# Performance work log

Hardware: AMD Instinct MI355X
Metric: run time of the kernel (lower is better)

The kernel has to match this reference:

```python
import jax, jax.numpy as jnp
import numpy as np

TOKEN_SELF_ATTN_VALUE = -5e4  # reformer_pytorch constant for masking self-attention
BUCKET_SIZE = 64
N_HASHES = 4
HEADS = 8


def look_one_back(x):
    # concat each chunk with the previous chunk along the within-chunk axis (axis=2)
    prev = jnp.concatenate([x[:, -1:], x[:, :-1]], axis=1)
    return jnp.concatenate([prev, x], axis=2)


def lsh_attention(qk, v, rotations):
    # qk, v: (b*h, t, dh); rotations: (dh, n_hashes, n_buckets//2)
    bh, seqlen, dim = qk.shape
    n_buckets = seqlen // BUCKET_SIZE
    # --- LSH bucket hashing via random rotations ---
    rotated = jnp.einsum('btf,fhi->bhti', qk, rotations)            # (bh, H, t, nb/2)
    rotated = jnp.concatenate([rotated, -rotated], axis=-1)          # (bh, H, t, nb)
    buckets = jnp.argmax(rotated, axis=-1)                           # (bh, H, t)
    offsets = (jnp.arange(N_HASHES) * n_buckets)[None, :, None]
    buckets = (buckets + offsets).reshape(bh, N_HASHES * seqlen)
    # --- stable sort tokens by (bucket, position) ---
    ticker = jnp.arange(N_HASHES * seqlen)
    buckets_and_t = seqlen * buckets + (ticker % seqlen)[None, :]
    sticker = jnp.argsort(buckets_and_t, axis=-1)                    # sorted ticker
    undo_sort = jnp.argsort(sticker, axis=-1)
    st = sticker % seqlen                                            # original positions
    sqk = jnp.take_along_axis(qk, st[..., None], axis=1)
    sv = jnp.take_along_axis(v, st[..., None], axis=1)
    # --- chunk into n_hashes*n_buckets chunks of bucket_size tokens ---
    n_chunks = N_HASHES * n_buckets
    bq_t = st.reshape(bh, n_chunks, -1)
    bqk = sqk.reshape(bh, n_chunks, -1, dim)
    bv = sv.reshape(bh, n_chunks, -1, dim)
    bq = bqk
    bk = bqk / jnp.maximum(jnp.linalg.norm(bqk, axis=-1, keepdims=True), 1e-12)
    bk = look_one_back(bk)
    bv = look_one_back(bv)
    bkv_t = look_one_back(bq_t)
    # --- chunked attention with one-chunk lookback ---
    dots = jnp.einsum('bcie,bcje->bcij', bq, bk) * (dim ** -0.5)     # (bh, nc, bs, 2*bs)
    dots = jnp.where(bq_t[:, :, :, None] == bkv_t[:, :, None, :], TOKEN_SELF_ATTN_VALUE, dots)
    dots_lse = jax.nn.logsumexp(dots, axis=-1, keepdims=True)
    probs = jnp.exp(dots - dots_lse)
    bo = jnp.einsum('bcij,bcje->bcie', probs, bv)
    so = bo.reshape(bh, N_HASHES * seqlen, dim)
    slogits = dots_lse.reshape(bh, N_HASHES * seqlen)
    # --- unsort and combine hash rounds weighted by logsumexp ---
    o = jnp.take_along_axis(so, undo_sort[..., None], axis=1)
    logits = jnp.take_along_axis(slogits, undo_sort, axis=1)
    o = o.reshape(bh, N_HASHES, seqlen, dim)
    logits = logits.reshape(bh, N_HASHES, seqlen, 1)
    w = jnp.exp(logits - jax.nn.logsumexp(logits, axis=1, keepdims=True))
    return jnp.sum(o * w, axis=1)


def _forward(queries, Wqk, Wv, Wo, bo, rotations):
    B, N, C = queries.shape
    m = BUCKET_SIZE * 2
    if N % m != 0:  # fit_length: zero-pad to multiple of bucket_size*2 (static)
        pad = m - N % m
        x = jnp.concatenate([queries, jnp.zeros((B, pad, C), queries.dtype)], axis=1)
    else:
        x = queries
    T = x.shape[1]
    dh = C // HEADS
    qk = jnp.einsum('btc,cf->btf', x, Wqk).reshape(B, T, HEADS, dh).transpose(0, 2, 1, 3).reshape(B * HEADS, T, dh)
    v = jnp.einsum('btc,cf->btf', x, Wv).reshape(B, T, HEADS, dh).transpose(0, 2, 1, 3).reshape(B * HEADS, T, dh)
    out = lsh_attention(qk, v, rotations)
    out = out.reshape(B, HEADS, T, dh).transpose(0, 2, 1, 3).reshape(B, T, C)
    out = jnp.einsum('btc,cf->btf', out, Wo) + bo
    return out[:, :N]


def setup_inputs() -> dict:
    key = jax.random.key(0)
    ks = jax.random.split(key, 7)
    B, N, C = 4, 4096, 512
    dh = C // HEADS
    n_buckets = N // BUCKET_SIZE  # 64
    return {
        'queries': jax.random.normal(ks[0], (B, N, C), jnp.float32),
        'keys': jax.random.normal(ks[1], (B, N, C), jnp.float32),
        'values': jax.random.normal(ks[2], (B, N, C), jnp.float32),
        'attn_mask': jnp.zeros((1,), jnp.bool_),
        'tau': 1,
        'delta': 1,
        'Wqk': jax.random.normal(ks[3], (C, C), jnp.float32) / np.float32(np.sqrt(C)),
        'Wv': jax.random.normal(ks[4], (C, C), jnp.float32) / np.float32(np.sqrt(C)),
        'Wo': jax.random.normal(ks[5], (C, C), jnp.float32) / np.float32(np.sqrt(C)),
        'bo': jnp.zeros((C,), jnp.float32),
        'rotations': jax.random.normal(ks[6], (dh, N_HASHES, n_buckets // 2), jnp.float32),
    }


def reference(queries, keys, values, attn_mask, tau, delta, Wqk, Wv, Wo, bo, rotations):
    # keys/values/attn_mask/tau/delta are accepted but unused, matching the torch module
    return _forward(queries, Wqk, Wv, Wo, bo, rotations)
```

## Files before the change

kernel.cpp:

```cpp
#include <hip/hip_runtime.h>
#include <hip/hip_bf16.h>
#include <cstdint>
#include <cstddef>

#define LSEQ   4096
#define DHD    64
#define NHASH  4
#define CDIM   512
#define NBH    32
#define MROWS  16384
#define NCHUNK 256

typedef __attribute__((ext_vector_type(8))) short short8;
typedef __attribute__((ext_vector_type(4))) float f32x4;
typedef __attribute__((ext_vector_type(2))) float f32x2;

__device__ inline uint32_t f2bf(float f) {
  uint32_t u = __float_as_uint(f);
  return (u + 0x7FFFu + ((u >> 16) & 1u)) >> 16;
}
__device__ inline float bf2f(uint32_t h) { return __uint_as_float(h << 16); }
__device__ inline void split2(float f, uint32_t& hi, uint32_t& lo) {
  hi = f2bf(f);
  lo = f2bf(f - bf2f(hi));
}
__device__ inline uint32_t cvtpk_bf16(float a, float b) {
  uint32_t r;
  asm("v_cvt_pk_bf16_f32 %0, %1, %2" : "=v"(r) : "v"(a), "v"(b));
  return r;
}
__device__ inline short8 ldsK(const uint16_t* p) {
  union { uint2 u[2]; short8 s; } t;
  t.u[0] = *reinterpret_cast<const uint2*>(p);
  t.u[1] = *reinterpret_cast<const uint2*>(p + 4);
  return t.s;
}

__global__ __launch_bounds__(256) void prep_kernel(
    const float* __restrict__ X, const float* __restrict__ Wv,
    const float* __restrict__ Wo,
    uint16_t* __restrict__ X0, uint16_t* __restrict__ X1,
    uint16_t* __restrict__ wvT0, uint16_t* __restrict__ wvT1,
    uint16_t* __restrict__ woT_hi, uint16_t* __restrict__ woT_lo)
{
  __shared__ float Ts[32][33];
  const int bid = blockIdx.x, tid = threadIdx.x;
  if (bid < 8192) {
    size_t i = ((size_t)bid * 256 + tid) * 4;
    float4 v = *reinterpret_cast<const float4*>(X + i);
    uint32_t h01 = cvtpk_bf16(v.x, v.y);
    uint32_t h23 = cvtpk_bf16(v.z, v.w);
    float r0 = v.x - __uint_as_float(h01 << 16);
    float r1 = v.y - __uint_as_float(h01 & 0xffff0000u);
    float r2 = v.z - __uint_as_float(h23 << 16);
    float r3 = v.w - __uint_as_float(h23 & 0xffff0000u);
    uint2 hw = {h01, h23};
    uint2 lw = {cvtpk_bf16(r0, r1), cvtpk_bf16(r2, r3)};
    *reinterpret_cast<uint2*>(X0 + i) = hw;
    *reinterpret_cast<uint2*>(X1 + i) = lw;
  } else if (bid < 9216) {
    int idx = (bid - 8192) * 256 + tid;
    int k = idx >> 9, n = idx & 511;
    uint32_t hi, lo;
    split2(Wo[idx], hi, lo);
    woT_hi[n * 512 + k] = (uint16_t)hi;
    woT_lo[n * 512 + k] = (uint16_t)lo;
  } else {
    int wb = bid - 9216;
    const int k0 = (wb >> 4) * 32, n0 = (wb & 15) * 32;
#pragma unroll
    for (int i = 0; i < 4; i++) {
      int flat = i * 256 + tid;
      int r = flat >> 5, c = flat & 31;
      Ts[r][c] = Wv[(size_t)(k0 + r) * 512 + n0 + c];
    }
    __syncthreads();
#pragma unroll
    for (int i = 0; i < 4; i++) {
      int flat = i * 256 + tid;
      int nr = flat >> 5, kc = flat & 31;
      uint32_t h, l;
      split2(Ts[kc][nr], h, l);
      size_t idx = (size_t)(n0 + nr) * 512 + k0 + kc;
      wvT0[idx] = (uint16_t)h;
      wvT1[idx] = (uint16_t)l;
    }
  }
}

__global__ __launch_bounds__(256) void gemm_qk_kernel(
    const float* __restrict__ X, const float* __restrict__ Wqk,
    float* __restrict__ qk, uint16_t* __restrict__ qkhi,
    uint16_t* __restrict__ qklo, float* __restrict__ invn_g)
{
  const int m0 = blockIdx.x * 128;
  const int n0 = blockIdx.y * 128;
  __shared__ float As[32][132];
  __shared__ float Bs[32][132];
  const int tid = threadIdx.x;
  const int r = tid >> 4, c = tid & 15;
  f32x2 acc2[8][4];
#pragma unroll
  for (int i = 0; i < 8; i++)
#pragma unroll
    for (int j = 0; j < 4; j++) acc2[i][j] = {0.f, 0.f};

  const int arow = tid >> 3;
  const int ac4  = tid & 7;
  const int brow = tid >> 5;
  const int bc4  = tid & 31;

  for (int kb = 0; kb < CDIM; kb += 32) {
#pragma unroll
    for (int rr = 0; rr < 4; rr++) {
      int m = arow + rr * 32;
      float4 av = *reinterpret_cast<const float4*>(&X[(size_t)(m0 + m) * CDIM + kb + ac4 * 4]);
      As[ac4 * 4 + 0][m] = av.x;
      As[ac4 * 4 + 1][m] = av.y;
      As[ac4 * 4 + 2][m] = av.z;
      As[ac4 * 4 + 3][m] = av.w;
    }
#pragma unroll
    for (int rr = 0; rr < 4; rr++) {
      int kk = brow + rr * 8;
      *reinterpret_cast<float4*>(&Bs[kk][bc4 * 4]) =
          *reinterpret_cast<const float4*>(&Wqk[(size_t)(kb + kk) * CDIM + n0 + bc4 * 4]);
    }
    __syncthreads();
#pragma unroll
    for (int k = 0; k < 32; k++) {
      float4 a0 = *reinterpret_cast<const float4*>(&As[k][r * 8]);
      float4 a1 = *reinterpret_cast<const float4*>(&As[k][r * 8 + 4]);
      float4 b0 = *reinterpret_cast<const float4*>(&Bs[k][c * 8]);
      float4 b1 = *reinterpret_cast<const float4*>(&Bs[k][c * 8 + 4]);
      float am[8] = {a0.x, a0.y, a0.z, a0.w, a1.x, a1.y, a1.z, a1.w};
      f32x2 bp[4] = {{b0.x, b0.y}, {b0.z, b0.w}, {b1.x, b1.y}, {b1.z, b1.w}};
#pragma unroll
      for (int i = 0; i < 8; i++) {
        f32x2 av = {am[i], am[i]};
#pragma unroll
        for (int jp = 0; jp < 4; jp++)
          acc2[i][jp] += av * bp[jp];
      }
    }
    __syncthreads();
  }
  const int head = (n0 >> 6) + (c >> 3);
#pragma unroll
  for (int ii = 0; ii < 8; ii++) {
    int m = m0 + r * 8 + ii;
    int b = m >> 12, t = m & 4095;
    size_t base = ((size_t)(b * 8 + head) * LSEQ + t) * DHD + (c & 7) * 8;
    float vals[8] = {acc2[ii][0][0], acc2[ii][0][1], acc2[ii][1][0], acc2[ii][1][1],
                     acc2[ii][2][0], acc2[ii][2][1], acc2[ii][3][0], acc2[ii][3][1]};
    *reinterpret_cast<float4*>(&qk[base]) = {vals[0], vals[1], vals[2], vals[3]};
    *reinterpret_cast<float4*>(&qk[base + 4]) = {vals[4], vals[5], vals[6], vals[7]};
    uint32_t hw[4], lw[4];
#pragma unroll
    for (int p = 0; p < 4; p++) {
      float x = vals[2 * p], y = vals[2 * p + 1];
      uint32_t h = cvtpk_bf16(x, y);
      float rx = x - __uint_as_float(h << 16);
      float ry = y - __uint_as_float(h & 0xffff0000u);
      hw[p] = h;
      lw[p] = cvtpk_bf16(rx, ry);
    }
    *reinterpret_cast<uint2*>(&qkhi[base]) = {hw[0], hw[1]};
    *reinterpret_cast<uint2*>(&qkhi[base + 4]) = {hw[2], hw[3]};
    *reinterpret_cast<uint2*>(&qklo[base]) = {lw[0], lw[1]};
    *reinterpret_cast<uint2*>(&qklo[base + 4]) = {lw[2], lw[3]};
    float ss = 0.f;
#pragma unroll
    for (int j = 0; j < 8; j++) ss += vals[j] * vals[j];
    ss += __shfl_xor(ss, 1, 64);
    ss += __shfl_xor(ss, 2, 64);
    ss += __shfl_xor(ss, 4, 64);
    if ((c & 7) == 0)
      invn_g[(size_t)(b * 8 + head) * LSEQ + t] = 1.0f / fmaxf(sqrtf(ss), 1e-12f);
  }
}

__global__ __launch_bounds__(512) void gemm_v_mfma_kernel(
    const uint16_t* __restrict__ X0g, const uint16_t* __restrict__ X1g,
    const uint16_t* __restrict__ Wv0, const uint16_t* __restrict__ Wv1,
    uint16_t* __restrict__ vhi)
{
  __shared__ __align__(16) uint16_t Xs[2 * 128 * 40];
  __shared__ __align__(16) uint16_t Ws[2 * 128 * 40];
  const int tid = threadIdx.x;
  const int m0 = blockIdx.x * 128;
  const int n0 = blockIdx.y * 128;
  const int lane = tid & 63, w = tid >> 6;
  const int l16 = lane & 15, lg = lane >> 4;

  f32x4 acc[8];
#pragma unroll
  for (int nt = 0; nt < 8; nt++) acc[nt] = {0.f, 0.f, 0.f, 0.f};

  const int srow = tid >> 3;
  const int sch = (tid & 7) * 4;

  for (int kb = 0; kb < CDIM; kb += 32) {
#pragma unroll
    for (int i = 0; i < 4; i++) {
      int p = i >> 1;
      int row = (i & 1) * 64 + srow;
      const uint16_t* xg = (p == 0) ? X0g : X1g;
      const uint16_t* wg = (p == 0) ? Wv0 : Wv1;
      *reinterpret_cast<uint2*>(Xs + p * 5120 + row * 40 + sch) =
          *reinterpret_cast<const uint2*>(xg + (size_t)(m0 + row) * 512 + kb + sch);
      *reinterpret_cast<uint2*>(Ws + p * 5120 + row * 40 + sch) =
          *reinterpret_cast<const uint2*>(wg + (size_t)(n0 + row) * 512 + kb + sch);
    }
    __syncthreads();

    const int abase = (w * 16 + l16) * 40 + lg * 8;
    short8 a0 = *reinterpret_cast<const short8*>(Xs + abase);
    short8 a1 = *reinterpret_cast<const short8*>(Xs + 5120 + abase);
#pragma unroll
    for (int nt = 0; nt < 8; nt++) {
      int bbase = (nt * 16 + l16) * 40 + lg * 8;
      short8 b0 = *reinterpret_cast<const short8*>(Ws + bbase);
      short8 b1 = *reinterpret_cast<const short8*>(Ws + 5120 + bbase);
      acc[nt] = __builtin_amdgcn_mfma_f32_16x16x32_bf16(a0, b0, acc[nt], 0, 0, 0);
      acc[nt] = __builtin_amdgcn_mfma_f32_16x16x32_bf16(a1, b0, acc[nt], 0, 0, 0);
      acc[nt] = __builtin_amdgcn_mfma_f32_16x16x32_bf16(a0, b1, acc[nt], 0, 0, 0);
    }
    __syncthreads();
  }

#pragma unroll
  for (int rr = 0; rr < 4; rr++) {
    int mg = m0 + w * 16 + lg * 4 + rr;
    int b = mg >> 12, t = mg & 4095;
#pragma unroll
    for (int nt = 0; nt < 8; nt++) {
      int head = (n0 >> 6) + (nt >> 2);
      size_t base = ((size_t)(b * 8 + head) * LSEQ + t) * DHD + (nt & 3) * 16 + l16;
      vhi[base] = (uint16_t)cvtpk_bf16(acc[nt][rr], acc[nt][rr]);
    }
  }
}

__global__ __launch_bounds__(256) void hash_kernel(
    const float* __restrict__ qk, const float* __restrict__ rot,
    int* __restrict__ buckets)
{
  __shared__ float rotT[128][68];
  const int tid = threadIdx.x;
  for (int idx = tid; idx < 64 * 128; idx += 256) {
    int f = idx >> 7, hi = idx & 127;
    rotT[hi][f] = rot[idx];
  }
  __syncthreads();
  const int bh = blockIdx.y;
  const int t = blockIdx.x * 256 + tid;
  float4 row4[16];
  const float* src = &qk[((size_t)bh * LSEQ + t) * DHD];
#pragma unroll
  for (int i = 0; i < 16; i++) row4[i] = reinterpret_cast<const float4*>(src)[i];

  int* bout = &buckets[(size_t)bh * NHASH * LSEQ];
  for (int h = 0; h < NHASH; h++) {
    float rc[32];
    float best = -3.0e38f;
    int bidx = 0;
#pragma unroll 4
    for (int i = 0; i < 32; i++) {
      const float* rr = &rotT[h * 32 + i][0];
      float a = 0.f;
#pragma unroll
      for (int f4 = 0; f4 < 16; f4++) {
        float4 rv = reinterpret_cast<const float4*>(rr)[f4];
        a += row4[f4].x * rv.x + row4[f4].y * rv.y + row4[f4].z * rv.z + row4[f4].w * rv.w;
      }
      rc[i] = a;
      if (a > best) { best = a; bidx = i; }
    }
#pragma unroll
    for (int i = 0; i < 32; i++) {
      float nv = -rc[i];
      if (nv > best) { best = nv; bidx = 32 + i; }
    }
    bout[h * LSEQ + t] = bidx;
  }
}

__global__ __launch_bounds__(256) void sort_kernel(
    const int* __restrict__ buckets, int* __restrict__ st)
{
  __shared__ int hist[64][64];
  const int h = blockIdx.x, bh = blockIdx.y;
  const int tid = threadIdx.x;
  const int* bk = &buckets[((size_t)bh * NHASH + h) * LSEQ];

  for (int i = tid; i < 64 * 64; i += 256) (&hist[0][0])[i] = 0;
  __syncthreads();
  for (int t = tid; t < LSEQ; t += 256) {
    int b = bk[t];
    atomicAdd(&hist[t >> 6][b], 1);
  }
  __syncthreads();
  if (tid < 64) {
    int tot = 0;
    for (int s = 0; s < 64; s++) tot += hist[s][tid];
    int vsc = tot;
    for (int off = 1; off < 64; off <<= 1) {
      int nv = __shfl_up(vsc, off, 64);
      if (tid >= off) vsc += nv;
    }
    int run = h * LSEQ + (vsc - tot);
    for (int s = 0; s < 64; s++) {
      int tmp = hist[s][tid];
      hist[s][tid] = run;
      run += tmp;
    }
  }
  __syncthreads();
  const int wave = tid >> 6, lane = tid & 63;
  for (int si = 0; si < 16; si++) {
    int seg = wave * 16 + si;
    int pos = seg * 64 + lane;
    int b = bk[pos];
    int rank = 0;
    for (int k = 0; k < 64; k++) {
      int bb = __shfl(b, k, 64);
      rank += (bb == b && k < lane) ? 1 : 0;
    }
    int dest = hist[seg][b] + rank;
    st[(size_t)bh * (NHASH * LSEQ) + dest] = pos;
  }
}

__global__ __launch_bounds__(256) void attn_kernel(
    const uint16_t* __restrict__ qkhi, const uint16_t* __restrict__ qklo,
    const uint16_t* __restrict__ vhi, const float* __restrict__ invn_g,
    const int* __restrict__ st, uint16_t* __restrict__ o,
    float* __restrict__ lse_out)
{
  __shared__ __align__(16) uint8_t smem[53248];
  uint16_t* Khi  = (uint16_t*)smem;
  uint16_t* Klo  = Khi + 128 * 68;
  uint16_t* Vthi = (uint16_t*)(smem + 34816);
  float*    invn = (float*)(smem + 52224);
  int*      kpos = (int*)(smem + 52736);
  uint32_t* P32  = (uint32_t*)smem;

  const int lin = blockIdx.y * 256 + blockIdx.x;
  const int xcd = lin & 7, sidx = lin >> 3;
  const int bh = (xcd << 2) | (sidx >> 8);
  const int cchunk = sidx & 255;

  const int tid = threadIdx.x;
  const int prev = (cchunk + NCHUNK - 1) & (NCHUNK - 1);
  const int* stb = &st[(size_t)bh * (NHASH * LSEQ)];
  const int h = cchunk >> 6;

  if (tid < 128) {
    int kp = (tid < 64) ? stb[prev * 64 + tid] : stb[cchunk * 64 + (tid - 64)];
    kpos[tid] = kp;
    invn[tid] = invn_g[(size_t)bh * LSEQ + kp];
  }
  __syncthreads();

  {
    const int d4 = tid & 15, rbase = tid >> 4;
    const uint16_t* qhb = qkhi + (size_t)bh * LSEQ * DHD;
    const uint16_t* qlb = qklo + (size_t)bh * LSEQ * DHD;
#pragma unroll
    for (int it = 0; it < 8; it++) {
      int row = rbase + it * 16;
      size_t src = (size_t)kpos[row] * DHD + d4 * 4;
      *reinterpret_cast<uint2*>(Khi + row * 68 + d4 * 4) =
          *reinterpret_cast<const uint2*>(qhb + src);
      *reinterpret_cast<uint2*>(Klo + row * 68 + d4 * 4) =
          *reinterpret_cast<const uint2*>(qlb + src);
    }
  }
  {
    const int d4 = tid & 15, jg0 = tid >> 4;
    const uint16_t* vb = vhi + (size_t)bh * LSEQ * DHD;
#pragma unroll
    for (int half = 0; half < 2; half++) {
      int jg = jg0 + half * 16;
      uint2 vr[4];
#pragma unroll
      for (int s = 0; s < 4; s++)
        vr[s] = *reinterpret_cast<const uint2*>(vb + (size_t)kpos[jg * 4 + s] * DHD + d4 * 4);
#pragma unroll
      for (int i = 0; i < 4; i++) {
        int d = d4 * 4 + i;
        uint32_t e0 = (((i & 2) ? vr[0].y : vr[0].x) >> ((i & 1) * 16)) & 0xffffu;
        uint32_t e1 = (((i & 2) ? vr[1].y : vr[1].x) >> ((i & 1) * 16)) & 0xffffu;
        uint32_t e2 = (((i & 2) ? vr[2].y : vr[2].x) >> ((i & 1) * 16)) & 0xffffu;
        uint32_t e3 = (((i & 2) ? vr[3].y : vr[3].x) >> ((i & 1) * 16)) & 0xffffu;
        uint2 outw = {e0 | (e1 << 16), e2 | (e3 << 16)};
        int cpr = (jg >> 1) ^ (d & 15);
        *reinterpret_cast<uint2*>(Vthi + d * 128 + cpr * 8 + (jg & 1) * 4) = outw;
      }
    }
  }
  __syncthreads();

  const int lane = tid & 63, w = tid >> 6;
  const int l16 = lane & 15, lg = lane >> 4;

  f32x4 acc[8];
#pragma unroll
  for (int nt = 0; nt < 8; nt++) acc[nt] = {0.f, 0.f, 0.f, 0.f};

#pragma unroll
  for (int ks = 0; ks < 2; ks++) {
    int aoff = (64 + w * 16 + l16) * 68 + ks * 32 + lg * 8;
    short8 a_hi = ldsK(Khi + aoff);
    short8 a_lo = ldsK(Klo + aoff);
#pragma unroll
    for (int nt = 0; nt < 8; nt++) {
      int boff = (nt * 16 + l16) * 68 + ks * 32 + lg * 8;
      short8 b_hi = ldsK(Khi + boff);
      short8 b_lo = ldsK(Klo + boff);
      acc[nt] = __builtin_amdgcn_mfma_f32_16x16x32_bf16(a_hi, b_hi, acc[nt], 0, 0, 0);
      acc[nt] = __builtin_amdgcn_mfma_f32_16x16x32_bf16(a_lo, b_hi, acc[nt], 0, 0, 0);
      acc[nt] = __builtin_amdgcn_mfma_f32_16x16x32_bf16(a_hi, b_lo, acc[nt], 0, 0, 0);
    }
  }

  float invc[8]; int kpc[8];
#pragma unroll
  for (int nt = 0; nt < 8; nt++) {
    invc[nt] = invn[nt * 16 + l16] * 0.125f;
    kpc[nt] = kpos[nt * 16 + l16];
  }
  float pll[4];
#pragma unroll
  for (int r = 0; r < 4; r++) {
    int q = w * 16 + lg * 4 + r;
    int qp = kpos[64 + q];
    float mm = -3.0e38f;
#pragma unroll
    for (int nt = 0; nt < 8; nt++) {
      float s = acc[nt][r] * invc[nt];
      if (qp == kpc[nt]) s = -5e4f;
      acc[nt][r] = s;
      mm = fmaxf(mm, s);
    }
    mm = fmaxf(mm, __shfl_xor(mm, 1, 64));
    mm = fmaxf(mm, __shfl_xor(mm, 2, 64));
    mm = fmaxf(mm, __shfl_xor(mm, 4, 64));
    mm = fmaxf(mm, __shfl_xor(mm, 8, 64));
    float ll = 0.f;
#pragma unroll
    for (int nt = 0; nt < 8; nt++) {
      float p = __expf(acc[nt][r] - mm);
      acc[nt][r] = p;
      ll += p;
    }
    ll += __shfl_xor(ll, 1, 64);
    ll += __shfl_xor(ll, 2, 64);
    ll += __shfl_xor(ll, 4, 64);
    ll += __shfl_xor(ll, 8, 64);
    if (l16 == 0)
      lse_out[(size_t)bh * (NHASH * LSEQ) + h * LSEQ + qp] = mm + __logf(ll);
    pll[r] = 1.0f / ll;
  }
  __syncthreads();

#pragma unroll
  for (int r = 0; r < 4; r++) {
    int q = w * 16 + lg * 4 + r;
#pragma unroll
    for (int nt = 0; nt < 8; nt++) {
      float p = acc[nt][r];
      uint32_t t1 = cvtpk_bf16(p, p);
      float res = p - __uint_as_float(t1 << 16);
      P32[q * 132 + nt * 16 + l16] = cvtpk_bf16(p, res);
    }
  }

  f32x4 oacc[4];
#pragma unroll
  for (int nt = 0; nt < 4; nt++) oacc[nt] = {0.f, 0.f, 0.f, 0.f};

#pragma unroll
  for (int ks = 0; ks < 4; ks++) {
    const uint32_t* pr = P32 + (w * 16 + l16) * 132 + ks * 32 + lg * 8;
    uint4 ua = *reinterpret_cast<const uint4*>(pr);
    uint4 ub = *reinterpret_cast<const uint4*>(pr + 4);
    uint32_t u[8] = {ua.x, ua.y, ua.z, ua.w, ub.x, ub.y, ub.z, ub.w};
    union { uint32_t w4[4]; short8 s8; } ph, pl;
#pragma unroll
    for (int k2 = 0; k2 < 4; k2++) {
      ph.w4[k2] = (u[2 * k2] & 0xffffu) | (u[2 * k2 + 1] << 16);
      pl.w4[k2] = (u[2 * k2] >> 16) | (u[2 * k2 + 1] & 0xffff0000u);
    }
    const int cc = ks * 4 + lg;
#pragma unroll
    for (int nt = 0; nt < 4; nt++) {
      int voff = (nt * 16 + l16) * 128 + ((cc ^ l16) & 15) * 8;
      short8 v_hi = *reinterpret_cast<const short8*>(Vthi + voff);
      oacc[nt] = __builtin_amdgcn_mfma_f32_16x16x32_bf16(ph.s8, v_hi, oacc[nt], 0, 0, 0);
      oacc[nt] = __builtin_amdgcn_mfma_f32_16x16x32_bf16(pl.s8, v_hi, oacc[nt], 0, 0, 0);
    }
  }

  {
    uint16_t* ob = o + ((size_t)bh * (NHASH * LSEQ) + (size_t)h * LSEQ) * DHD;
#pragma unroll
    for (int r = 0; r < 4; r++) {
      int q = w * 16 + lg * 4 + r;
      int qp = kpos[64 + q];
      float s = pll[r];
#pragma unroll
      for (int nt = 0; nt < 4; nt++) {
        float v = oacc[nt][r] * s;
        ob[(size_t)qp * DHD + nt * 16 + l16] = (uint16_t)cvtpk_bf16(v, v);
      }
    }
  }
}

__global__ __launch_bounds__(256) void combine_kernel(
    const uint16_t* __restrict__ o, const float* __restrict__ lse,
    uint16_t* __restrict__ comb_hi, uint16_t* __restrict__ comb_lo)
{
  int gid = blockIdx.x * 4 + (threadIdx.x >> 6);
  int lane = threadIdx.x & 63;
  int bh = gid >> 12;
  int pos = gid & 4095;
  const float* lb = &lse[(size_t)bh * (NHASH * LSEQ) + pos];
  float l0 = lb[0], l1 = lb[LSEQ], l2 = lb[2 * LSEQ], l3 = lb[3 * LSEQ];
  float m = fmaxf(fmaxf(l0, l1), fmaxf(l2, l3));
  float w0 = __expf(l0 - m), w1 = __expf(l1 - m), w2 = __expf(l2 - m), w3 = __expf(l3 - m);
  float inv = 1.0f / (w0 + w1 + w2 + w3);
  const uint16_t* ob = &o[((size_t)bh * (NHASH * LSEQ) + pos) * DHD];
  float val = (w0 * bf2f(ob[lane]) + w1 * bf2f(ob[(size_t)LSEQ * DHD + lane]) +
               w2 * bf2f(ob[(size_t)2 * LSEQ * DHD + lane]) +
               w3 * bf2f(ob[(size_t)3 * LSEQ * DHD + lane])) * inv;
  int b = bh >> 3, head = bh & 7;
  size_t idx = ((size_t)(b * LSEQ + pos)) * CDIM + head * DHD + lane;
  uint32_t hw = cvtpk_bf16(val, val);
  float res = val - __uint_as_float(hw << 16);
  comb_hi[idx] = (uint16_t)hw;
  comb_lo[idx] = (uint16_t)cvtpk_bf16(res, res);
}

__global__ __launch_bounds__(256) void gemm_out_kernel(
    const uint16_t* __restrict__ Ahi_g, const uint16_t* __restrict__ Alo_g,
    const uint16_t* __restrict__ Bhi_g, const uint16_t* __restrict__ Blo_g,
    const float* __restrict__ bias, float* __restrict__ out)
{
  __shared__ __align__(16) uint16_t Ah[128 * 40];
  __shared__ __align__(16) uint16_t Al[128 * 40];
  __shared__ __align__(16) uint16_t Bh[128 * 40];
  __shared__ __align__(16) uint16_t Bl[128 * 40];
  const int tid = threadIdx.x;
  const int m0 = blockIdx.x * 128, n0 = blockIdx.y * 128;
  const int lane = tid & 63, w = tid >> 6;
  const int l16 = lane & 15, lg = lane >> 4;
  const int mq = w >> 1, nq = w & 1;
  f32x4 acc[4][4];
#pragma unroll
  for (int i = 0; i < 4; i++)
#pragma unroll
    for (int j = 0; j < 4; j++) acc[i][j] = {0.f, 0.f, 0.f, 0.f};

  const int srow = tid >> 1, sh = tid & 1;
  for (int kb = 0; kb < CDIM; kb += 32) {
    {
      const uint4* sa_h = (const uint4*)(Ahi_g + (size_t)(m0 + srow) * CDIM + kb + sh * 16);
      const uint4* sa_l = (const uint4*)(Alo_g + (size_t)(m0 + srow) * CDIM + kb + sh * 16);
      const uint4* sb_h = (const uint4*)(Bhi_g + (size_t)(n0 + srow) * CDIM + kb + sh * 16);
      const uint4* sb_l = (const uint4*)(Blo_g + (size_t)(n0 + srow) * CDIM + kb + sh * 16);
      uint4* da_h = (uint4*)(Ah + srow * 40 + sh * 16);
      uint4* da_l = (uint4*)(Al + srow * 40 + sh * 16);
      uint4* db_h = (uint4*)(Bh + srow * 40 + sh * 16);
      uint4* db_l = (uint4*)(Bl + srow * 40 + sh * 16);
      da_h[0] = sa_h[0]; da_h[1] = sa_h[1];
      da_l[0] = sa_l[0]; da_l[1] = sa_l[1];
      db_h[0] = sb_h[0]; db_h[1] = sb_h[1];
      db_l[0] = sb_l[0]; db_l[1] = sb_l[1];
    }
    __syncthreads();
    short8 fa_h[4], fa_l[4], fb_h[4], fb_l[4];
#pragma unroll
    for (int mt = 0; mt < 4; mt++) {
      int ao = (mq * 64 + mt * 16 + l16) * 40 + lg * 8;
      fa_h[mt] = *reinterpret_cast<const short8*>(Ah + ao);
      fa_l[mt] = *reinterpret_cast<const short8*>(Al + ao);
    }
#pragma unroll
    for (int nt = 0; nt < 4; nt++) {
      int bo_ = (nq * 64 + nt * 16 + l16) * 40 + lg * 8;
      fb_h[nt] = *reinterpret_cast<const short8*>(Bh + bo_);
      fb_l[nt] = *reinterpret_cast<const short8*>(Bl + bo_);
    }
#pragma unroll
    for (int mt = 0; mt < 4; mt++)
#pragma unroll
      for (int nt = 0; nt < 4; nt++) {
        acc[mt][nt] = __builtin_amdgcn_mfma_f32_16x16x32_bf16(fa_h[mt], fb_h[nt], acc[mt][nt], 0, 0, 0);
        acc[mt][nt] = __builtin_amdgcn_mfma_f32_16x16x32_bf16(fa_l[mt], fb_h[nt], acc[mt][nt], 0, 0, 0);
        acc[mt][nt] = __builtin_amdgcn_mfma_f32_16x16x32_bf16(fa_h[mt], fb_l[nt], acc[mt][nt], 0, 0, 0);
      }
    __syncthreads();
  }
#pragma unroll
  for (int nt = 0; nt < 4; nt++) {
    int n = n0 + nq * 64 + nt * 16 + l16;
    float bv = bias[n];
#pragma unroll
    for (int mt = 0; mt < 4; mt++) {
#pragma unroll
      for (int rr = 0; rr < 4; rr++) {
        int m = m0 + mq * 64 + mt * 16 + lg * 4 + rr;
        out[(size_t)m * CDIM + n] = acc[mt][nt][rr] + bv;
      }
    }
  }
}

extern "C" void kernel_launch(void* const* d_in, const int* in_sizes, int n_in,
                              void* d_out, int out_size, void* d_ws, size_t ws_size,
                              hipStream_t stream) {
  (void)in_sizes; (void)n_in; (void)out_size; (void)ws_size;
  const float* X    = (const float*)d_in[0];
  const float* Wqk  = (const float*)d_in[6];
  const float* Wv   = (const float*)d_in[7];
  const float* Wo   = (const float*)d_in[8];
  const float* bo   = (const float*)d_in[9];
  const float* rot  = (const float*)d_in[10];

  uint8_t* W = (uint8_t*)d_ws;
  float*    qk      = (float*)(W + 0);
  uint16_t* obuf    = (uint16_t*)(W + 33554432);
  uint16_t* qkhi    = (uint16_t*)(W + 100663296);
  uint16_t* qklo    = (uint16_t*)(W + 117440512);
  uint16_t* vhi     = (uint16_t*)(W + 134217728);
  int*      buckets = (int*)(W + 150994944);
  int*      st      = (int*)(W + 153092096);
  float*    lse     = (float*)(W + 155189248);
  float*    invn_g  = (float*)(W + 157286400);
  uint16_t* woT_hi  = (uint16_t*)(W + 157810688);
  uint16_t* woT_lo  = (uint16_t*)(W + 158334976);
  uint16_t* wvT0    = (uint16_t*)(W + 158859264);
  uint16_t* wvT1    = (uint16_t*)(W + 159383552);
  uint16_t* x0      = (uint16_t*)(W + 33554432);
  uint16_t* x1      = (uint16_t*)(W + 50331648);
  uint16_t* comb_hi = (uint16_t*)(W + 0);
  uint16_t* comb_lo = (uint16_t*)(W + 16777216);

  hipLaunchKernelGGL(prep_kernel, dim3(9472), dim3(256), 0, stream,
                     X, Wv, Wo, x0, x1, wvT0, wvT1, woT_hi, woT_lo);
  hipLaunchKernelGGL(gemm_qk_kernel, dim3(128, 4), dim3(256), 0, stream,
                     X, Wqk, qk, qkhi, qklo, invn_g);
  hipLaunchKernelGGL(gemm_v_mfma_kernel, dim3(128, 4), dim3(512), 0, stream,
                     x0, x1, wvT0, wvT1, vhi);
  hipLaunchKernelGGL(hash_kernel, dim3(16, 32), dim3(256), 0, stream,
                     qk, rot, buckets);
  hipLaunchKernelGGL(sort_kernel, dim3(4, 32), dim3(256), 0, stream,
                     buckets, st);
  hipLaunchKernelGGL(attn_kernel, dim3(256, 32), dim3(256), 0, stream,
                     qkhi, qklo, vhi, invn_g, st, obuf, lse);
  hipLaunchKernelGGL(combine_kernel, dim3(32768), dim3(256), 0, stream,
                     obuf, lse, comb_hi, comb_lo);
  hipLaunchKernelGGL(gemm_out_kernel, dim3(128, 4), dim3(256), 0, stream,
                     comb_hi, comb_lo, woT_hi, woT_lo, bo, (float*)d_out);
}
```

Measured before the change: 439.6 us.

## Double thread count and register-prefetch tiles in fp32 QK projection GEMM

The fp32 QK projection GEMM now runs 512 threads per block, each computing an 8x4 micro-tile instead of 8x8. The next K-slice of X and Wqk is prefetched into registers while the current shared-memory tile is being consumed. The epilogue and the row-norm shuffle reduction are adjusted to the new 16-lane-per-head layout. This trades per-thread work for more waves and overlaps global loads with compute, but each thread gets less FMA reuse per shared-memory load.

```diff
diff --git a/kernel.cpp b/kernel.cpp
--- a/kernel.cpp
+++ b/kernel.cpp
@@ -88,7 +88,7 @@
   }
 }
 
-__global__ __launch_bounds__(256) void gemm_qk_kernel(
+__global__ __launch_bounds__(512) void gemm_qk_kernel(
     const float* __restrict__ X, const float* __restrict__ Wqk,
     float* __restrict__ qk, uint16_t* __restrict__ qkhi,
     uint16_t* __restrict__ qklo, float* __restrict__ invn_g)
@@ -98,84 +98,84 @@
   __shared__ float As[32][132];
   __shared__ float Bs[32][132];
   const int tid = threadIdx.x;
-  const int r = tid >> 4, c = tid & 15;
-  f32x2 acc2[8][4];
-#pragma unroll
-  for (int i = 0; i < 8; i++)
-#pragma unroll
-    for (int j = 0; j < 4; j++) acc2[i][j] = {0.f, 0.f};
-
-  const int arow = tid >> 3;
-  const int ac4  = tid & 7;
-  const int brow = tid >> 5;
-  const int bc4  = tid & 31;
+  const int r = tid >> 5, c = tid & 31;
+  f32x2 acc2[8][2];
+#pragma unroll
+  for (int i = 0; i < 8; i++) {
+    acc2[i][0] = {0.f, 0.f};
+    acc2[i][1] = {0.f, 0.f};
+  }
+
+  const int arow = tid >> 2;
+  const int ak   = (tid & 3) * 4;
+  const int brow = tid >> 4;
+  const int bn   = (tid & 15) * 4;
+
+  float4 pa[2], pb[2];
+#pragma unroll
+  for (int rr = 0; rr < 2; rr++) {
+    pa[rr] = *reinterpret_cast<const float4*>(&X[(size_t)(m0 + arow) * CDIM + ak + rr * 16]);
+    pb[rr] = *reinterpret_cast<const float4*>(&Wqk[(size_t)brow * CDIM + n0 + bn + rr * 64]);
+  }
 
   for (int kb = 0; kb < CDIM; kb += 32) {
 #pragma unroll
-    for (int rr = 0; rr < 4; rr++) {
-      int m = arow + rr * 32;
-      float4 av = *reinterpret_cast<const float4*>(&X[(size_t)(m0 + m) * CDIM + kb + ac4 * 4]);
-      As[ac4 * 4 + 0][m] = av.x;
-      As[ac4 * 4 + 1][m] = av.y;
-      As[ac4 * 4 + 2][m] = av.z;
-      As[ac4 * 4 + 3][m] = av.w;
-    }
-#pragma unroll
-    for (int rr = 0; rr < 4; rr++) {
-      int kk = brow + rr * 8;
-      *reinterpret_cast<float4*>(&Bs[kk][bc4 * 4]) =
-          *reinterpret_cast<const float4*>(&Wqk[(size_t)(kb + kk) * CDIM + n0 + bc4 * 4]);
+    for (int rr = 0; rr < 2; rr++) {
+      As[ak + rr * 16 + 0][arow] = pa[rr].x;
+      As[ak + rr * 16 + 1][arow] = pa[rr].y;
+      As[ak + rr * 16 + 2][arow] = pa[rr].z;
+      As[ak + rr * 16 + 3][arow] = pa[rr].w;
+      *reinterpret_cast<float4*>(&Bs[brow][bn + rr * 64]) = pb[rr];
     }
     __syncthreads();
+    if (kb + 32 < CDIM) {
+#pragma unroll
+      for (int rr = 0; rr < 2; rr++) {
+        pa[rr] = *reinterpret_cast<const float4*>(
+            &X[(size_t)(m0 + arow) * CDIM + kb + 32 + ak + rr * 16]);
+        pb[rr] = *reinterpret_cast<const float4*>(
+            &Wqk[(size_t)(kb + 32 + brow) * CDIM + n0 + bn + rr * 64]);
+      }
+    }
 #pragma unroll
     for (int k = 0; k < 32; k++) {
       float4 a0 = *reinterpret_cast<const float4*>(&As[k][r * 8]);
       float4 a1 = *reinterpret_cast<const float4*>(&As[k][r * 8 + 4]);
-      float4 b0 = *reinterpret_cast<const float4*>(&Bs[k][c * 8]);
-      float4 b1 = *reinterpret_cast<const float4*>(&Bs[k][c * 8 + 4]);
+      float4 b  = *reinterpret_cast<const float4*>(&Bs[k][c * 4]);
       float am[8] = {a0.x, a0.y, a0.z, a0.w, a1.x, a1.y, a1.z, a1.w};
-      f32x2 bp[4] = {{b0.x, b0.y}, {b0.z, b0.w}, {b1.x, b1.y}, {b1.z, b1.w}};
+      f32x2 b01 = {b.x, b.y};
+      f32x2 b23 = {b.z, b.w};
 #pragma unroll
       for (int i = 0; i < 8; i++) {
         f32x2 av = {am[i], am[i]};
-#pragma unroll
-        for (int jp = 0; jp < 4; jp++)
-          acc2[i][jp] += av * bp[jp];
+        acc2[i][0] += av * b01;
+        acc2[i][1] += av * b23;
       }
     }
     __syncthreads();
   }
-  const int head = (n0 >> 6) + (c >> 3);
+  const int head = (n0 >> 6) + (c >> 4);
 #pragma unroll
   for (int ii = 0; ii < 8; ii++) {
     int m = m0 + r * 8 + ii;
     int b = m >> 12, t = m & 4095;
-    size_t base = ((size_t)(b * 8 + head) * LSEQ + t) * DHD + (c & 7) * 8;
-    float vals[8] = {acc2[ii][0][0], acc2[ii][0][1], acc2[ii][1][0], acc2[ii][1][1],
-                     acc2[ii][2][0], acc2[ii][2][1], acc2[ii][3][0], acc2[ii][3][1]};
-    *reinterpret_cast<float4*>(&qk[base]) = {vals[0], vals[1], vals[2], vals[3]};
-    *reinterpret_cast<float4*>(&qk[base + 4]) = {vals[4], vals[5], vals[6], vals[7]};
-    uint32_t hw[4], lw[4];
-#pragma unroll
-    for (int p = 0; p < 4; p++) {
-      float x = vals[2 * p], y = vals[2 * p + 1];
-      uint32_t h = cvtpk_bf16(x, y);
-      float rx = x - __uint_as_float(h << 16);
-      float ry = y - __uint_as_float(h & 0xffff0000u);
-      hw[p] = h;
-      lw[p] = cvtpk_bf16(rx, ry);
-    }
-    *reinterpret_cast<uint2*>(&qkhi[base]) = {hw[0], hw[1]};
-    *reinterpret_cast<uint2*>(&qkhi[base + 4]) = {hw[2], hw[3]};
-    *reinterpret_cast<uint2*>(&qklo[base]) = {lw[0], lw[1]};
-    *reinterpret_cast<uint2*>(&qklo[base + 4]) = {lw[2], lw[3]};
-    float ss = 0.f;
-#pragma unroll
-    for (int j = 0; j < 8; j++) ss += vals[j] * vals[j];
+    size_t base = ((size_t)(b * 8 + head) * LSEQ + t) * DHD + (c & 15) * 4;
+    float4 ov = {acc2[ii][0][0], acc2[ii][0][1], acc2[ii][1][0], acc2[ii][1][1]};
+    *reinterpret_cast<float4*>(&qk[base]) = ov;
+    uint32_t h0 = cvtpk_bf16(ov.x, ov.y);
+    uint32_t h1 = cvtpk_bf16(ov.z, ov.w);
+    float r0 = ov.x - __uint_as_float(h0 << 16);
+    float r1 = ov.y - __uint_as_float(h0 & 0xffff0000u);
+    float r2 = ov.z - __uint_as_float(h1 << 16);
+    float r3 = ov.w - __uint_as_float(h1 & 0xffff0000u);
+    *reinterpret_cast<uint2*>(&qkhi[base]) = {h0, h1};
+    *reinterpret_cast<uint2*>(&qklo[base]) = {cvtpk_bf16(r0, r1), cvtpk_bf16(r2, r3)};
+    float ss = ov.x * ov.x + ov.y * ov.y + ov.z * ov.z + ov.w * ov.w;
     ss += __shfl_xor(ss, 1, 64);
     ss += __shfl_xor(ss, 2, 64);
     ss += __shfl_xor(ss, 4, 64);
-    if ((c & 7) == 0)
+    ss += __shfl_xor(ss, 8, 64);
+    if ((c & 15) == 0)
       invn_g[(size_t)(b * 8 + head) * LSEQ + t] = 1.0f / fmaxf(sqrtf(ss), 1e-12f);
   }
 }
@@ -651,7 +651,7 @@
 
   hipLaunchKernelGGL(prep_kernel, dim3(9472), dim3(256), 0, stream,
                      X, Wv, Wo, x0, x1, wvT0, wvT1, woT_hi, woT_lo);
-  hipLaunchKernelGGL(gemm_qk_kernel, dim3(128, 4), dim3(256), 0, stream,
+  hipLaunchKernelGGL(gemm_qk_kernel, dim3(128, 4), dim3(512), 0, stream,
                      X, Wqk, qk, qkhi, qklo, invn_g);
   hipLaunchKernelGGL(gemm_v_mfma_kernel, dim3(128, 4), dim3(512), 0, stream,
                      x0, x1, wvT0, wvT1, vhi);
```

After: 443.8 us. No clear change (+1.0%).

## Retile fp32 QK projection GEMM to 64-row tiles with per-wave column slices

Applied to the files above, without the earlier changes.

The FP32 QK projection GEMM drops its 128x128 tile for a 64x128 tile. Each wave now owns 32 output columns, and each lane owns one row, reading a broadcast B row and a padded A element from shared memory. Doubling the grid raises block count and occupancy. The row norm is now reduced through a small shared-memory partial array instead of shuffles. In exchange, reuse drops: each thread does 16 FMAs per A load but needs 8 float4 B reads per k, and per-lane stores are strided by 64 floats, so output writes are less coalesced.

```diff
diff --git a/kernel.cpp b/kernel.cpp
--- a/kernel.cpp
+++ b/kernel.cpp
@@ -93,90 +93,93 @@
     float* __restrict__ qk, uint16_t* __restrict__ qkhi,
     uint16_t* __restrict__ qklo, float* __restrict__ invn_g)
 {
-  const int m0 = blockIdx.x * 128;
+  __shared__ float As[64 * 33];
+  __shared__ float Bs[32 * 132];
+  __shared__ float part[4][64];
+  const int tid = threadIdx.x;
+  const int m0 = blockIdx.x * 64;
   const int n0 = blockIdx.y * 128;
-  __shared__ float As[32][132];
-  __shared__ float Bs[32][132];
-  const int tid = threadIdx.x;
-  const int r = tid >> 4, c = tid & 15;
-  f32x2 acc2[8][4];
-#pragma unroll
-  for (int i = 0; i < 8; i++)
-#pragma unroll
-    for (int j = 0; j < 4; j++) acc2[i][j] = {0.f, 0.f};
-
-  const int arow = tid >> 3;
-  const int ac4  = tid & 7;
-  const int brow = tid >> 5;
-  const int bc4  = tid & 31;
+  const int lane = tid & 63;
+  const int w = __builtin_amdgcn_readfirstlane(tid >> 6);
+  const int wn = w * 32;
+
+  f32x2 acc2[16];
+#pragma unroll
+  for (int j = 0; j < 16; j++) acc2[j] = {0.f, 0.f};
+
+  const int arow = tid >> 2;
+  const int akc  = (tid & 3) * 8;
+  const int bk   = tid >> 3;
+  const int bnc  = (tid & 7) * 16;
 
   for (int kb = 0; kb < CDIM; kb += 32) {
-#pragma unroll
-    for (int rr = 0; rr < 4; rr++) {
-      int m = arow + rr * 32;
-      float4 av = *reinterpret_cast<const float4*>(&X[(size_t)(m0 + m) * CDIM + kb + ac4 * 4]);
-      As[ac4 * 4 + 0][m] = av.x;
-      As[ac4 * 4 + 1][m] = av.y;
-      As[ac4 * 4 + 2][m] = av.z;
-      As[ac4 * 4 + 3][m] = av.w;
-    }
-#pragma unroll
-    for (int rr = 0; rr < 4; rr++) {
-      int kk = brow + rr * 8;
-      *reinterpret_cast<float4*>(&Bs[kk][bc4 * 4]) =
-          *reinterpret_cast<const float4*>(&Wqk[(size_t)(kb + kk) * CDIM + n0 + bc4 * 4]);
-    }
     __syncthreads();
-#pragma unroll
+    {
+      float4 x0 = *reinterpret_cast<const float4*>(&X[(size_t)(m0 + arow) * CDIM + kb + akc]);
+      float4 x1 = *reinterpret_cast<const float4*>(&X[(size_t)(m0 + arow) * CDIM + kb + akc + 4]);
+      float* dst = &As[arow * 33 + akc];
+      dst[0] = x0.x; dst[1] = x0.y; dst[2] = x0.z; dst[3] = x0.w;
+      dst[4] = x1.x; dst[5] = x1.y; dst[6] = x1.z; dst[7] = x1.w;
+    }
+    {
+      const float* srcb = &Wqk[(size_t)(kb + bk) * CDIM + n0 + bnc];
+      float* dstb = &Bs[bk * 132 + bnc];
+#pragma unroll
+      for (int q = 0; q < 4; q++)
+        *reinterpret_cast<float4*>(dstb + q * 4) =
+            *reinterpret_cast<const float4*>(srcb + q * 4);
+    }
+    __syncthreads();
+#pragma unroll 8
     for (int k = 0; k < 32; k++) {
-      float4 a0 = *reinterpret_cast<const float4*>(&As[k][r * 8]);
-      float4 a1 = *reinterpret_cast<const float4*>(&As[k][r * 8 + 4]);
-      float4 b0 = *reinterpret_cast<const float4*>(&Bs[k][c * 8]);
-      float4 b1 = *reinterpret_cast<const float4*>(&Bs[k][c * 8 + 4]);
-      float am[8] = {a0.x, a0.y, a0.z, a0.w, a1.x, a1.y, a1.z, a1.w};
-      f32x2 bp[4] = {{b0.x, b0.y}, {b0.z, b0.w}, {b1.x, b1.y}, {b1.z, b1.w}};
-#pragma unroll
-      for (int i = 0; i < 8; i++) {
-        f32x2 av = {am[i], am[i]};
-#pragma unroll
-        for (int jp = 0; jp < 4; jp++)
-          acc2[i][jp] += av * bp[jp];
-      }
-    }
-    __syncthreads();
-  }
-  const int head = (n0 >> 6) + (c >> 3);
-#pragma unroll
-  for (int ii = 0; ii < 8; ii++) {
-    int m = m0 + r * 8 + ii;
-    int b = m >> 12, t = m & 4095;
-    size_t base = ((size_t)(b * 8 + head) * LSEQ + t) * DHD + (c & 7) * 8;
-    float vals[8] = {acc2[ii][0][0], acc2[ii][0][1], acc2[ii][1][0], acc2[ii][1][1],
-                     acc2[ii][2][0], acc2[ii][2][1], acc2[ii][3][0], acc2[ii][3][1]};
-    *reinterpret_cast<float4*>(&qk[base]) = {vals[0], vals[1], vals[2], vals[3]};
-    *reinterpret_cast<float4*>(&qk[base + 4]) = {vals[4], vals[5], vals[6], vals[7]};
-    uint32_t hw[4], lw[4];
-#pragma unroll
-    for (int p = 0; p < 4; p++) {
-      float x = vals[2 * p], y = vals[2 * p + 1];
-      uint32_t h = cvtpk_bf16(x, y);
-      float rx = x - __uint_as_float(h << 16);
-      float ry = y - __uint_as_float(h & 0xffff0000u);
-      hw[p] = h;
-      lw[p] = cvtpk_bf16(rx, ry);
-    }
-    *reinterpret_cast<uint2*>(&qkhi[base]) = {hw[0], hw[1]};
-    *reinterpret_cast<uint2*>(&qkhi[base + 4]) = {hw[2], hw[3]};
-    *reinterpret_cast<uint2*>(&qklo[base]) = {lw[0], lw[1]};
-    *reinterpret_cast<uint2*>(&qklo[base + 4]) = {lw[2], lw[3]};
-    float ss = 0.f;
-#pragma unroll
-    for (int j = 0; j < 8; j++) ss += vals[j] * vals[j];
-    ss += __shfl_xor(ss, 1, 64);
-    ss += __shfl_xor(ss, 2, 64);
-    ss += __shfl_xor(ss, 4, 64);
-    if ((c & 7) == 0)
-      invn_g[(size_t)(b * 8 + head) * LSEQ + t] = 1.0f / fmaxf(sqrtf(ss), 1e-12f);
+      float a = As[lane * 33 + k];
+      const float4* bq = reinterpret_cast<const float4*>(&Bs[k * 132 + wn]);
+      float4 b0 = bq[0], b1 = bq[1], b2 = bq[2], b3 = bq[3];
+      float4 b4 = bq[4], b5 = bq[5], b6 = bq[6], b7 = bq[7];
+      f32x2 av = {a, a};
+      acc2[0]  += av * f32x2{b0.x, b0.y};
+      acc2[1]  += av * f32x2{b0.z, b0.w};
+      acc2[2]  += av * f32x2{b1.x, b1.y};
+      acc2[3]  += av * f32x2{b1.z, b1.w};
+      acc2[4]  += av * f32x2{b2.x, b2.y};
+      acc2[5]  += av * f32x2{b2.z, b2.w};
+      acc2[6]  += av * f32x2{b3.x, b3.y};
+      acc2[7]  += av * f32x2{b3.z, b3.w};
+      acc2[8]  += av * f32x2{b4.x, b4.y};
+      acc2[9]  += av * f32x2{b4.z, b4.w};
+      acc2[10] += av * f32x2{b5.x, b5.y};
+      acc2[11] += av * f32x2{b5.z, b5.w};
+      acc2[12] += av * f32x2{b6.x, b6.y};
+      acc2[13] += av * f32x2{b6.z, b6.w};
+      acc2[14] += av * f32x2{b7.x, b7.y};
+      acc2[15] += av * f32x2{b7.z, b7.w};
+    }
+  }
+
+  const int nw = n0 + wn;
+  const int head = nw >> 6;
+  const int d0 = nw & 63;
+  const int m = m0 + lane;
+  const int b = m >> 12, t = m & 4095;
+  const size_t base = ((size_t)(b * 8 + head) * LSEQ + t) * DHD + d0;
+
+  float ss = 0.f;
+#pragma unroll
+  for (int j = 0; j < 16; j++) {
+    float x = acc2[j][0], y = acc2[j][1];
+    *reinterpret_cast<float2*>(&qk[base + 2 * j]) = {x, y};
+    uint32_t h = cvtpk_bf16(x, y);
+    float rx = x - __uint_as_float(h << 16);
+    float ry = y - __uint_as_float(h & 0xffff0000u);
+    reinterpret_cast<uint32_t*>(qkhi + base)[j] = h;
+    reinterpret_cast<uint32_t*>(qklo + base)[j] = cvtpk_bf16(rx, ry);
+    ss += x * x + y * y;
+  }
+  part[w][lane] = ss;
+  __syncthreads();
+  if ((w & 1) == 0) {
+    float tot = part[w][lane] + part[w + 1][lane];
+    invn_g[(size_t)(b * 8 + head) * LSEQ + t] = 1.0f / fmaxf(sqrtf(tot), 1e-12f);
   }
 }
 
@@ -651,7 +654,7 @@
 
   hipLaunchKernelGGL(prep_kernel, dim3(9472), dim3(256), 0, stream,
                      X, Wv, Wo, x0, x1, wvT0, wvT1, woT_hi, woT_lo);
-  hipLaunchKernelGGL(gemm_qk_kernel, dim3(128, 4), dim3(256), 0, stream,
+  hipLaunchKernelGGL(gemm_qk_kernel, dim3(256, 4), dim3(256), 0, stream,
                      X, Wqk, qk, qkhi, qklo, invn_g);
   hipLaunchKernelGGL(gemm_v_mfma_kernel, dim3(128, 4), dim3(512), 0, stream,
                      x0, x1, wvT0, wvT1, vhi);
```

Result: slower. 486.7 us (+10.7%).
